# Kernel optimization log

Hardware: AMD Instinct MI355X
Metric: run time of the kernel (lower is better)

Reference implementation:

```python
import jax, jax.numpy as jnp
import numpy as np
from jax import lax

ALPHA = 50.0
BN_EPS = 1e-5
L2_EPS = 1e-12

N, C, H, W = 32, 128, 128, 128
K = 64  # num_clusters


def _l2norm(v, axis):
    n = jnp.sqrt(jnp.sum(v * v, axis=axis, keepdims=True))
    return v / jnp.maximum(n, L2_EPS)


def setup_inputs() -> dict:
    key = jax.random.key(0)
    ks = jax.random.split(key, 4)
    x = jax.random.normal(ks[0], (N, C, H, W), dtype=jnp.float32)
    conv_w = jax.random.normal(ks[1], (C, C, 3, 3), dtype=jnp.float32) * 0.05
    bn_gamma = jnp.ones((C,), jnp.float32)
    bn_beta = jnp.zeros((C,), jnp.float32)
    bn_mean = jnp.zeros((C,), jnp.float32)
    bn_var = jnp.ones((C,), jnp.float32)
    # conv.weight in NetVLAD is centroids.permute(1,0): shape (dim, num_clusters)
    vlad_w = jax.random.normal(ks[2], (C, K), dtype=jnp.float32)
    vlad_b = jnp.zeros((K,), jnp.float32)  # initialized to zeros in _init_params
    return {"input": x, "conv_w": conv_w, "bn_gamma": bn_gamma, "bn_beta": bn_beta,
            "bn_mean": bn_mean, "bn_var": bn_var, "vlad_w": vlad_w, "vlad_b": vlad_b,
            "norm_flag": 1}


def reference(input, conv_w, bn_gamma, bn_beta, bn_mean, bn_var, vlad_w, vlad_b, norm_flag):
    # bottleneck_layer_2: conv3x3 stride2 pad1 (no bias) -> BN (eval form) -> ReLU
    f = lax.conv_general_dilated(input, conv_w, window_strides=(2, 2),
                                 padding=[(1, 1), (1, 1)],
                                 dimension_numbers=("NCHW", "OIHW", "NCHW"))
    inv = bn_gamma / jnp.sqrt(bn_var + BN_EPS)
    f = f * inv[None, :, None, None] + (bn_beta - bn_mean * inv)[None, :, None, None]
    f = jax.nn.relu(f)

    n, c, h, w = f.shape
    hw = h * w
    # normalize_input: L2 over channel dim
    xn = _l2norm(f, axis=1)
    xf = xn.reshape(n, c, hw)  # (N,C,HW)

    # soft assignment: x^T @ normalize(W, dim=0), bias added, softmax over clusters
    wn = _l2norm(vlad_w, axis=0)                     # (C,K)
    sa_ = jnp.einsum("nci,ck->nik", xf, wn)          # (N,HW,K)
    logits = jnp.swapaxes(sa_, 1, 2) + vlad_b[None, :, None]  # (N,K,HW)
    a = jax.nn.softmax(ALPHA * logits, axis=1)       # softmax over K

    # vlad_k = sum_i a_ki * x_i - (sum_i a_ki) * c_k  (c_k = vlad_w[:,k], unnormalized)
    asum = jnp.sum(a, axis=-1)                       # (N,K)
    vlad = jnp.einsum("nki,nci->nkc", a, xf) - asum[:, :, None] * vlad_w.T[None]  # (N,K,C)

    vlad = _l2norm(vlad, axis=2)                     # intra-normalization
    vlad = vlad.reshape(n, -1)
    vlad = _l2norm(vlad, axis=1)

    feature = jnp.swapaxes(xf, 1, 2)                 # (N,HW,C)
    soft_assign_out = jnp.swapaxes(sa_, 1, 2)        # (N,K,HW)
    return (vlad, soft_assign_out, feature)
```

## Files before the change

kernel.cpp:

```cpp
#include <hip/hip_runtime.h>

typedef short short8 __attribute__((ext_vector_type(8)));
typedef float floatx4 __attribute__((ext_vector_type(4)));

#define ALPHA 50.0f
#define BN_EPS 1e-5f

#define SA_BASE   262144L
#define FEAT_BASE 8650752L

#define T_OFF    0L
#define AW_OFF   0L
#define PART_OFF 50331648L
#define XNT_OFF  138444800L
#define WB_OFF   171999232L
#define WNA_OFF  172294144L
#define ASUM_OFF 172310528L

__device__ __forceinline__ unsigned short f2bf(float f) {
    unsigned u = __builtin_bit_cast(unsigned, f);
    u = u + 0x7FFFu + ((u >> 16) & 1u);
    return (unsigned short)(u >> 16);
}

__device__ __forceinline__ void gl_lds16(const void* g, void* l) {
    __builtin_amdgcn_global_load_lds(
        (const __attribute__((address_space(1))) unsigned int*)g,
        (__attribute__((address_space(3))) unsigned int*)l, 16, 0, 0);
}

__global__ __launch_bounds__(256) void k_prep(const float* __restrict__ conv_w,
                                              const float* __restrict__ vlad_w,
                                              unsigned short* __restrict__ wB,
                                              unsigned short* __restrict__ wnA,
                                              float* __restrict__ asum) {
    int b = blockIdx.x, t = threadIdx.x;
    if (b < 576) {
        int idx = b * 256 + t;
        int ci = idx & 127, co = (idx >> 7) & 127, tap = idx >> 14;
        float w = conv_w[(co * 128 + ci) * 9 + tap];
        wB[(tap * 128 + co) * 128 + ci] = f2bf(w);
    } else {
        if (t < 64) {
            int k = t;
            float s = 0.0f;
            for (int c = 0; c < 128; c++) { float w = vlad_w[c * 64 + k]; s += w * w; }
            float rs = 1.0f / fmaxf(sqrtf(s), 1e-12f);
            for (int c = 0; c < 128; c++) wnA[k * 128 + c] = f2bf(vlad_w[c * 64 + k] * rs);
        } else {
            for (int i = t - 64; i < 2048; i += 192) asum[i] = 0.0f;
        }
    }
}

__global__ __launch_bounds__(256) void k_border(unsigned short* __restrict__ T) {
    int n = blockIdx.x, t = threadIdx.x;
    uint4 z = make_uint4(0, 0, 0, 0);
    for (int i = t; i < 4128; i += 256) {
        long e;
        if (i < 2080) {
            int ix = i >> 4, oct = i & 15;
            e = (((long)n * 130 + 0) * 130 + ix) * 128 + oct * 8;
        } else {
            int j = i - 2080;
            int row = (j >> 4) + 1, oct = j & 15;
            e = (((long)n * 130 + row) * 130 + 0) * 128 + oct * 8;
        }
        *(uint4*)(T + e) = z;
    }
}

__global__ __launch_bounds__(256) void k_xform(const float* __restrict__ in,
                                               unsigned short* __restrict__ T) {
    int y = blockIdx.x, n = blockIdx.y, t = threadIdx.x;
    __shared__ float ls[64 * 133];
    for (int cc = 0; cc < 2; cc++) {
        __syncthreads();
        int ci0 = cc * 64;
#pragma unroll
        for (int i = 0; i < 8; i++) {
            int idx = i * 256 + t;
            int ci = idx >> 5, xq = idx & 31;
            float4 v = *(const float4*)(in + ((((long)n * 128 + ci0 + ci) * 128 + y) * 128 + xq * 4));
            *(float4*)(&ls[ci * 133 + xq * 4]) = v;
        }
        __syncthreads();
#pragma unroll
        for (int i = 0; i < 4; i++) {
            int idx = i * 256 + t;
            int x = idx >> 3, oct = idx & 7;
            short8 pk;
#pragma unroll
            for (int j = 0; j < 8; j++)
                pk[j] = (short)f2bf(ls[(oct * 8 + j) * 133 + x]);
            long e = (((long)n * 130 + y + 1) * 130 + (x + 1)) * 128 + ci0 + oct * 8;
            *(short8*)(T + e) = pk;
        }
    }
}

__global__ __launch_bounds__(256) void k_conv(const unsigned short* __restrict__ T,
                                              const unsigned short* __restrict__ wB,
                                              const float* __restrict__ gamma,
                                              const float* __restrict__ beta,
                                              const float* __restrict__ mean,
                                              const float* __restrict__ var,
                                              float* __restrict__ out,
                                              unsigned short* __restrict__ xnT) {
    int ypair = blockIdx.x, n = blockIdx.y;
    int t = threadIdx.x, lane = t & 63, w = t >> 6;
    int wm = w >> 1, wn = w & 1;
    int s = lane & 15, q = lane >> 4;
    int y0 = ypair * 2;

    __shared__ __align__(16) short lsA[20800];
    __shared__ float lsq[256];

    floatx4 acc[4][4];
#pragma unroll
    for (int a = 0; a < 4; a++)
#pragma unroll
        for (int b = 0; b < 4; b++) acc[a][b] = (floatx4){0.f, 0.f, 0.f, 0.f};

    const unsigned short* Tbase = T + (((long)n * 130 + 2 * y0) * 130) * 128;
    int bbase0 = (wn * 64 + s) * 128 + q * 8;

    for (int cc = 0; cc < 4; cc++) {
        int ci0 = cc * 32;
        const unsigned short* Tc = Tbase + ci0;
#pragma unroll
        for (int i = 0; i < 11; i++) {
            int f = i * 256 + t;
            short* lbase = &lsA[2048 * i + 512 * w];
            if (f < 2600) {
                int r = f / 520;
                int rem = f - r * 520;
                int p = rem >> 3;
                int o8 = (rem & 7) ^ (p & 7);
                int ix = 2 * p + (o8 >> 2);
                int oct = o8 & 3;
                gl_lds16(Tc + (((long)(r * 130 + ix)) << 7) + (oct << 3), lbase);
            }
        }
        __syncthreads();
#pragma unroll
        for (int tap = 0; tap < 9; tap++) {
            const int dy = tap / 3, dx = tap % 3;
            short8 af[4], bf[4];
#pragma unroll
            for (int tm = 0; tm < 4; tm++) {
                int x = tm * 16 + s;
                int p = x + (dx >> 1);
                int o8p = (((dx & 1) << 2) | q) ^ (p & 7);
                int r = 2 * wm + dy;
                af[tm] = *(const short8*)(&lsA[(((r * 65 + p) << 3) + o8p) << 3]);
            }
#pragma unroll
            for (int tn = 0; tn < 4; tn++)
                bf[tn] = *(const short8*)(wB + bbase0 + tap * 16384 + tn * 2048 + ci0);
#pragma unroll
            for (int tm = 0; tm < 4; tm++)
#pragma unroll
                for (int tn = 0; tn < 4; tn++)
                    acc[tm][tn] = __builtin_amdgcn_mfma_f32_16x16x32_bf16(af[tm], bf[tn], acc[tm][tn], 0, 0, 0);
        }
        __syncthreads();
    }

    float inv[4], bt[4];
#pragma unroll
    for (int tn = 0; tn < 4; tn++) {
        int co = wn * 64 + tn * 16 + s;
        inv[tn] = gamma[co] / sqrtf(var[co] + BN_EPS);
        bt[tn] = beta[co] - mean[co] * inv[tn];
    }
#pragma unroll
    for (int tm = 0; tm < 4; tm++)
#pragma unroll
        for (int tn = 0; tn < 4; tn++)
#pragma unroll
            for (int r = 0; r < 4; r++) {
                float f = acc[tm][tn][r] * inv[tn] + bt[tn];
                acc[tm][tn][r] = fmaxf(f, 0.0f);
            }
#pragma unroll
    for (int tm = 0; tm < 4; tm++)
#pragma unroll
        for (int r = 0; r < 4; r++) {
            float p = 0.f;
#pragma unroll
            for (int tn = 0; tn < 4; tn++) { float f = acc[tm][tn][r]; p += f * f; }
            p += __shfl_xor(p, 1); p += __shfl_xor(p, 2);
            p += __shfl_xor(p, 4); p += __shfl_xor(p, 8);
            if (s == 0) lsq[wn * 128 + wm * 64 + tm * 16 + q * 4 + r] = p;
        }
    __syncthreads();
    float scl[4][4];
#pragma unroll
    for (int tm = 0; tm < 4; tm++)
#pragma unroll
        for (int r = 0; r < 4; r++) {
            int m = wm * 64 + tm * 16 + q * 4 + r;
            float tot = lsq[m] + lsq[128 + m];
            scl[tm][r] = 1.0f / fmaxf(sqrtf(tot), 1e-12f);
        }
    short* lsT = lsA;
    long pixbase = (long)n * 4096 + y0 * 64;
#pragma unroll
    for (int tm = 0; tm < 4; tm++)
#pragma unroll
        for (int r = 0; r < 4; r++) {
            int m = wm * 64 + tm * 16 + q * 4 + r;
#pragma unroll
            for (int tn = 0; tn < 4; tn++) {
                int co = wn * 64 + tn * 16 + s;
                float xv = acc[tm][tn][r] * scl[tm][r];
                out[FEAT_BASE + (pixbase + m) * 128 + co] = xv;
                lsT[co * 136 + m] = (short)f2bf(xv);
            }
        }
    __syncthreads();
    {
        int co = t >> 1, mh = t & 1;
        long base = ((long)n * 128 + co) * 4096 + y0 * 64 + mh * 64;
#pragma unroll
        for (int o = 0; o < 8; o++) {
            short8 v = *(short8*)(&lsT[co * 136 + mh * 64 + o * 8]);
            *(short8*)(xnT + base + o * 8) = v;
        }
    }
}

__global__ __launch_bounds__(256) void k_sa(const float* __restrict__ feat,
                                            const unsigned short* __restrict__ wnA,
                                            const float* __restrict__ vlad_b,
                                            float* __restrict__ out,
                                            unsigned short* __restrict__ aout,
                                            float* __restrict__ asum) {
    int pt = blockIdx.x, n = blockIdx.y;
    int t = threadIdx.x, lane = t & 63, w = t >> 6;
    int s = lane & 15, q = lane >> 4;
    int pb = pt * 256 + w * 64;

    floatx4 acc[4][4];
#pragma unroll
    for (int a = 0; a < 4; a++)
#pragma unroll
        for (int b = 0; b < 4; b++) acc[a][b] = (floatx4){0.f, 0.f, 0.f, 0.f};

    const float* fb = feat + FEAT_BASE + (long)n * 4096 * 128;
#pragma unroll
    for (int kk = 0; kk < 4; kk++) {
        int c0 = kk * 32 + q * 8;
        short8 af[4], bf[4];
#pragma unroll
        for (int tm = 0; tm < 4; tm++)
            af[tm] = *(const short8*)(wnA + (tm * 16 + s) * 128 + c0);
#pragma unroll
        for (int tn = 0; tn < 4; tn++) {
            const float* p = fb + (long)(pb + tn * 16 + s) * 128 + c0;
            float4 v0 = *(const float4*)p;
            float4 v1 = *(const float4*)(p + 4);
            short8 bv;
            bv[0] = (short)f2bf(v0.x); bv[1] = (short)f2bf(v0.y);
            bv[2] = (short)f2bf(v0.z); bv[3] = (short)f2bf(v0.w);
            bv[4] = (short)f2bf(v1.x); bv[5] = (short)f2bf(v1.y);
            bv[6] = (short)f2bf(v1.z); bv[7] = (short)f2bf(v1.w);
            bf[tn] = bv;
        }
#pragma unroll
        for (int tm = 0; tm < 4; tm++)
#pragma unroll
            for (int tn = 0; tn < 4; tn++)
                acc[tm][tn] = __builtin_amdgcn_mfma_f32_16x16x32_bf16(af[tm], bf[tn], acc[tm][tn], 0, 0, 0);
    }
    long sabase = SA_BASE + (long)n * 64 * 4096;
#pragma unroll
    for (int tm = 0; tm < 4; tm++)
#pragma unroll
        for (int r = 0; r < 4; r++) {
            int k = tm * 16 + q * 4 + r;
#pragma unroll
            for (int tn = 0; tn < 4; tn++)
                out[sabase + (long)k * 4096 + pb + tn * 16 + s] = acc[tm][tn][r];
        }
    float bv[4][4];
#pragma unroll
    for (int tm = 0; tm < 4; tm++)
#pragma unroll
        for (int r = 0; r < 4; r++) bv[tm][r] = vlad_b[tm * 16 + q * 4 + r];
#pragma unroll
    for (int tn = 0; tn < 4; tn++) {
        float M = -1e30f;
#pragma unroll
        for (int tm = 0; tm < 4; tm++)
#pragma unroll
            for (int r = 0; r < 4; r++)
                M = fmaxf(M, ALPHA * (acc[tm][tn][r] + bv[tm][r]));
        M = fmaxf(M, __shfl_xor(M, 16)); M = fmaxf(M, __shfl_xor(M, 32));
        float S = 0.f;
#pragma unroll
        for (int tm = 0; tm < 4; tm++)
#pragma unroll
            for (int r = 0; r < 4; r++) {
                float p = expf(ALPHA * (acc[tm][tn][r] + bv[tm][r]) - M);
                acc[tm][tn][r] = p; S += p;
            }
        S += __shfl_xor(S, 16); S += __shfl_xor(S, 32);
        float rS = 1.0f / S;
#pragma unroll
        for (int tm = 0; tm < 4; tm++)
#pragma unroll
            for (int r = 0; r < 4; r++) acc[tm][tn][r] *= rS;
    }
    long abase = (long)n * 64 * 4096;
#pragma unroll
    for (int tm = 0; tm < 4; tm++)
#pragma unroll
        for (int r = 0; r < 4; r++) {
            int k = tm * 16 + q * 4 + r;
#pragma unroll
            for (int tn = 0; tn < 4; tn++)
                aout[abase + (long)k * 4096 + pb + tn * 16 + s] = f2bf(acc[tm][tn][r]);
            float p = acc[tm][0][r] + acc[tm][1][r] + acc[tm][2][r] + acc[tm][3][r];
            p += __shfl_xor(p, 1); p += __shfl_xor(p, 2);
            p += __shfl_xor(p, 4); p += __shfl_xor(p, 8);
            if (s == 0) atomicAdd(asum + n * 64 + k, p);
        }
}

__global__ __launch_bounds__(256) void k_vlad1(const unsigned short* __restrict__ aw,
                                               const unsigned short* __restrict__ xnT,
                                               float* __restrict__ part) {
    int ch = blockIdx.x, n = blockIdx.y;
    int t = threadIdx.x, lane = t & 63, w = t >> 6;
    int wm = w >> 1, wn = w & 1;
    int s = lane & 15, q = lane >> 4;

    floatx4 acc[2][4];
#pragma unroll
    for (int a = 0; a < 2; a++)
#pragma unroll
        for (int b = 0; b < 4; b++) acc[a][b] = (floatx4){0.f, 0.f, 0.f, 0.f};

    const unsigned short* ab = aw + (long)n * 64 * 4096;
    const unsigned short* xb = xnT + (long)n * 128 * 4096;
    int ibeg = ch * 256, iend = ibeg + 256;
    for (int i0 = ibeg; i0 < iend; i0 += 32) {
        short8 af[2], bf[4];
#pragma unroll
        for (int tm = 0; tm < 2; tm++)
            af[tm] = *(const short8*)(ab + (long)(wm * 32 + tm * 16 + s) * 4096 + i0 + q * 8);
#pragma unroll
        for (int tn = 0; tn < 4; tn++)
            bf[tn] = *(const short8*)(xb + (long)(wn * 64 + tn * 16 + s) * 4096 + i0 + q * 8);
#pragma unroll
        for (int tm = 0; tm < 2; tm++)
#pragma unroll
            for (int tn = 0; tn < 4; tn++)
                acc[tm][tn] = __builtin_amdgcn_mfma_f32_16x16x32_bf16(af[tm], bf[tn], acc[tm][tn], 0, 0, 0);
    }
    float* pb = part + ((long)n * 16 + ch) * 8192;
#pragma unroll
    for (int tm = 0; tm < 2; tm++)
#pragma unroll
        for (int r = 0; r < 4; r++) {
            int k = wm * 32 + tm * 16 + q * 4 + r;
#pragma unroll
            for (int tn = 0; tn < 4; tn++) {
                int c = wn * 64 + tn * 16 + s;
                pb[k * 128 + c] = acc[tm][tn][r];
            }
        }
}

__global__ __launch_bounds__(256) void k_vlad2(const float* __restrict__ part,
                                               const float* __restrict__ vlad_w,
                                               const float* __restrict__ asum,
                                               float* __restrict__ out) {
    int n = blockIdx.x;
    int t = threadIdx.x, lane = t & 63, w = t >> 6;
    __shared__ float lsq[128];
    __shared__ float gsq[4];

    float v[32];
    const float* pb = part + (long)n * 16 * 8192;
#pragma unroll
    for (int j = 0; j < 32; j++) {
        int e = j * 256 + t;
        float sacc = 0.f;
#pragma unroll
        for (int c8 = 0; c8 < 16; c8++) sacc += pb[c8 * 8192 + e];
        int k = e >> 7, c = e & 127;
        sacc -= asum[n * 64 + k] * vlad_w[c * 64 + k];
        v[j] = sacc;
        float p = sacc * sacc;
        p += __shfl_xor(p, 1); p += __shfl_xor(p, 2); p += __shfl_xor(p, 4);
        p += __shfl_xor(p, 8); p += __shfl_xor(p, 16); p += __shfl_xor(p, 32);
        if (lane == 0) lsq[j * 4 + w] = p;
    }
    __syncthreads();
    float gp = 0.f;
#pragma unroll
    for (int j = 0; j < 32; j++) {
        float tot = lsq[j * 4 + (w & 2)] + lsq[j * 4 + (w & 2) + 1];
        float sc = 1.0f / fmaxf(sqrtf(tot), 1e-12f);
        v[j] *= sc;
        gp += v[j] * v[j];
    }
    gp += __shfl_xor(gp, 1); gp += __shfl_xor(gp, 2); gp += __shfl_xor(gp, 4);
    gp += __shfl_xor(gp, 8); gp += __shfl_xor(gp, 16); gp += __shfl_xor(gp, 32);
    if (lane == 0) gsq[w] = gp;
    __syncthreads();
    float sc2 = 1.0f / fmaxf(sqrtf(gsq[0] + gsq[1] + gsq[2] + gsq[3]), 1e-12f);
#pragma unroll
    for (int j = 0; j < 32; j++)
        out[(long)n * 8192 + j * 256 + t] = v[j] * sc2;
}

extern "C" void kernel_launch(void* const* d_in, const int* in_sizes, int n_in,
                              void* d_out, int out_size, void* d_ws, size_t ws_size,
                              hipStream_t stream) {
    const float* input  = (const float*)d_in[0];
    const float* conv_w = (const float*)d_in[1];
    const float* gamma  = (const float*)d_in[2];
    const float* beta   = (const float*)d_in[3];
    const float* mean   = (const float*)d_in[4];
    const float* var    = (const float*)d_in[5];
    const float* vlad_w = (const float*)d_in[6];
    const float* vlad_b = (const float*)d_in[7];
    float* out = (float*)d_out;
    char* ws = (char*)d_ws;

    unsigned short* T   = (unsigned short*)(ws + T_OFF);
    unsigned short* aw  = (unsigned short*)(ws + AW_OFF);
    float* part         = (float*)(ws + PART_OFF);
    unsigned short* xnT = (unsigned short*)(ws + XNT_OFF);
    unsigned short* wB  = (unsigned short*)(ws + WB_OFF);
    unsigned short* wnA = (unsigned short*)(ws + WNA_OFF);
    float* asum         = (float*)(ws + ASUM_OFF);

    k_prep<<<577, 256, 0, stream>>>(conv_w, vlad_w, wB, wnA, asum);
    k_border<<<32, 256, 0, stream>>>(T);
    k_xform<<<dim3(128, 32), 256, 0, stream>>>(input, T);
    k_conv<<<dim3(32, 32), 256, 0, stream>>>(T, wB, gamma, beta, mean, var, out, xnT);
    k_sa<<<dim3(16, 32), 256, 0, stream>>>(out, wnA, vlad_b, out, aw, asum);
    k_vlad1<<<dim3(16, 32), 256, 0, stream>>>(aw, xnT, part);
    k_vlad2<<<32, 256, 0, stream>>>(part, vlad_w, asum, out);
}
```

Baseline: 610.8 us.

## Fuse soft-assignment and VLAD aggregation into conv kernel epilogue

The soft-assignment GEMM, softmax, asum accumulation and per-tile VLAD partial GEMM now run inside the conv kernel on the normalized features already held in LDS, replacing the separate k_sa and k_vlad1 kernels. This removes the global round trips for the feature reread, the bf16 assignment matrix and the transposed feature copy, along with two launches. In exchange the conv kernel uses more LDS and registers, which may lower occupancy, and the partial buffer doubles to 32 slices per image, so k_vlad2 does a longer reduction.

```diff
diff --git a/kernel.cpp b/kernel.cpp
--- a/kernel.cpp
+++ b/kernel.cpp
@@ -10,9 +10,7 @@
 #define FEAT_BASE 8650752L
 
 #define T_OFF    0L
-#define AW_OFF   0L
-#define PART_OFF 50331648L
-#define XNT_OFF  138444800L
+#define PART_OFF 138444800L
 #define WB_OFF   171999232L
 #define WNA_OFF  172294144L
 #define ASUM_OFF 172310528L
@@ -105,15 +103,18 @@
                                               const float* __restrict__ beta,
                                               const float* __restrict__ mean,
                                               const float* __restrict__ var,
+                                              const unsigned short* __restrict__ wnA,
+                                              const float* __restrict__ vlad_b,
                                               float* __restrict__ out,
-                                              unsigned short* __restrict__ xnT) {
+                                              float* __restrict__ part,
+                                              float* __restrict__ asum) {
     int ypair = blockIdx.x, n = blockIdx.y;
     int t = threadIdx.x, lane = t & 63, w = t >> 6;
     int wm = w >> 1, wn = w & 1;
     int s = lane & 15, q = lane >> 4;
     int y0 = ypair * 2;
 
-    __shared__ __align__(16) short lsA[20800];
+    __shared__ __align__(16) short lsA[26112];
     __shared__ float lsq[256];
 
     floatx4 acc[4][4];
@@ -220,157 +221,120 @@
             }
         }
     __syncthreads();
-    {
-        int co = t >> 1, mh = t & 1;
-        long base = ((long)n * 128 + co) * 4096 + y0 * 64 + mh * 64;
-#pragma unroll
-        for (int o = 0; o < 8; o++) {
-            short8 v = *(short8*)(&lsT[co * 136 + mh * 64 + o * 8]);
-            *(short8*)(xnT + base + o * 8) = v;
-        }
-    }
-}
-
-__global__ __launch_bounds__(256) void k_sa(const float* __restrict__ feat,
-                                            const unsigned short* __restrict__ wnA,
-                                            const float* __restrict__ vlad_b,
-                                            float* __restrict__ out,
-                                            unsigned short* __restrict__ aout,
-                                            float* __restrict__ asum) {
-    int pt = blockIdx.x, n = blockIdx.y;
-    int t = threadIdx.x, lane = t & 63, w = t >> 6;
-    int s = lane & 15, q = lane >> 4;
-    int pb = pt * 256 + w * 64;
-
-    floatx4 acc[4][4];
+
+    floatx4 acc2[4][2];
 #pragma unroll
     for (int a = 0; a < 4; a++)
 #pragma unroll
-        for (int b = 0; b < 4; b++) acc[a][b] = (floatx4){0.f, 0.f, 0.f, 0.f};
-
-    const float* fb = feat + FEAT_BASE + (long)n * 4096 * 128;
+        for (int b = 0; b < 2; b++) acc2[a][b] = (floatx4){0.f, 0.f, 0.f, 0.f};
+    int pixw = w * 32;
 #pragma unroll
     for (int kk = 0; kk < 4; kk++) {
         int c0 = kk * 32 + q * 8;
-        short8 af[4], bf[4];
+        short8 af2[4], bf2[2];
 #pragma unroll
         for (int tm = 0; tm < 4; tm++)
-            af[tm] = *(const short8*)(wnA + (tm * 16 + s) * 128 + c0);
-#pragma unroll
-        for (int tn = 0; tn < 4; tn++) {
-            const float* p = fb + (long)(pb + tn * 16 + s) * 128 + c0;
-            float4 v0 = *(const float4*)p;
-            float4 v1 = *(const float4*)(p + 4);
+            af2[tm] = *(const short8*)(wnA + (tm * 16 + s) * 128 + c0);
+#pragma unroll
+        for (int tn = 0; tn < 2; tn++) {
+            int pix = pixw + tn * 16 + s;
             short8 bv;
-            bv[0] = (short)f2bf(v0.x); bv[1] = (short)f2bf(v0.y);
-            bv[2] = (short)f2bf(v0.z); bv[3] = (short)f2bf(v0.w);
-            bv[4] = (short)f2bf(v1.x); bv[5] = (short)f2bf(v1.y);
-            bv[6] = (short)f2bf(v1.z); bv[7] = (short)f2bf(v1.w);
-            bf[tn] = bv;
+#pragma unroll
+            for (int j = 0; j < 8; j++)
+                bv[j] = lsT[(c0 + j) * 136 + pix];
+            bf2[tn] = bv;
         }
 #pragma unroll
         for (int tm = 0; tm < 4; tm++)
 #pragma unroll
-            for (int tn = 0; tn < 4; tn++)
-                acc[tm][tn] = __builtin_amdgcn_mfma_f32_16x16x32_bf16(af[tm], bf[tn], acc[tm][tn], 0, 0, 0);
-    }
-    long sabase = SA_BASE + (long)n * 64 * 4096;
+            for (int tn = 0; tn < 2; tn++)
+                acc2[tm][tn] = __builtin_amdgcn_mfma_f32_16x16x32_bf16(af2[tm], bf2[tn], acc2[tm][tn], 0, 0, 0);
+    }
+    long sabase = SA_BASE + (long)n * 262144 + (long)(y0 * 64 + pixw);
 #pragma unroll
     for (int tm = 0; tm < 4; tm++)
 #pragma unroll
         for (int r = 0; r < 4; r++) {
             int k = tm * 16 + q * 4 + r;
 #pragma unroll
-            for (int tn = 0; tn < 4; tn++)
-                out[sabase + (long)k * 4096 + pb + tn * 16 + s] = acc[tm][tn][r];
-        }
-    float bv[4][4];
-#pragma unroll
-    for (int tm = 0; tm < 4; tm++)
-#pragma unroll
-        for (int r = 0; r < 4; r++) bv[tm][r] = vlad_b[tm * 16 + q * 4 + r];
-#pragma unroll
-    for (int tn = 0; tn < 4; tn++) {
+            for (int tn = 0; tn < 2; tn++)
+                out[sabase + (long)k * 4096 + tn * 16 + s] = acc2[tm][tn][r];
+        }
+    float bv2[4][4];
+#pragma unroll
+    for (int tm = 0; tm < 4; tm++)
+#pragma unroll
+        for (int r = 0; r < 4; r++) bv2[tm][r] = vlad_b[tm * 16 + q * 4 + r];
+#pragma unroll
+    for (int tn = 0; tn < 2; tn++) {
         float M = -1e30f;
 #pragma unroll
         for (int tm = 0; tm < 4; tm++)
 #pragma unroll
             for (int r = 0; r < 4; r++)
-                M = fmaxf(M, ALPHA * (acc[tm][tn][r] + bv[tm][r]));
+                M = fmaxf(M, ALPHA * (acc2[tm][tn][r] + bv2[tm][r]));
         M = fmaxf(M, __shfl_xor(M, 16)); M = fmaxf(M, __shfl_xor(M, 32));
         float S = 0.f;
 #pragma unroll
         for (int tm = 0; tm < 4; tm++)
 #pragma unroll
             for (int r = 0; r < 4; r++) {
-                float p = expf(ALPHA * (acc[tm][tn][r] + bv[tm][r]) - M);
-                acc[tm][tn][r] = p; S += p;
+                float p = expf(ALPHA * (acc2[tm][tn][r] + bv2[tm][r]) - M);
+                acc2[tm][tn][r] = p; S += p;
             }
         S += __shfl_xor(S, 16); S += __shfl_xor(S, 32);
         float rS = 1.0f / S;
 #pragma unroll
         for (int tm = 0; tm < 4; tm++)
 #pragma unroll
-            for (int r = 0; r < 4; r++) acc[tm][tn][r] *= rS;
-    }
-    long abase = (long)n * 64 * 4096;
+            for (int r = 0; r < 4; r++) acc2[tm][tn][r] *= rS;
+    }
+    short* lsAa = lsA + 17408;
 #pragma unroll
     for (int tm = 0; tm < 4; tm++)
 #pragma unroll
         for (int r = 0; r < 4; r++) {
             int k = tm * 16 + q * 4 + r;
 #pragma unroll
-            for (int tn = 0; tn < 4; tn++)
-                aout[abase + (long)k * 4096 + pb + tn * 16 + s] = f2bf(acc[tm][tn][r]);
-            float p = acc[tm][0][r] + acc[tm][1][r] + acc[tm][2][r] + acc[tm][3][r];
+            for (int tn = 0; tn < 2; tn++)
+                lsAa[k * 136 + pixw + tn * 16 + s] = (short)f2bf(acc2[tm][tn][r]);
+            float p = acc2[tm][0][r] + acc2[tm][1][r];
             p += __shfl_xor(p, 1); p += __shfl_xor(p, 2);
             p += __shfl_xor(p, 4); p += __shfl_xor(p, 8);
             if (s == 0) atomicAdd(asum + n * 64 + k, p);
         }
-}
-
-__global__ __launch_bounds__(256) void k_vlad1(const unsigned short* __restrict__ aw,
-                                               const unsigned short* __restrict__ xnT,
-                                               float* __restrict__ part) {
-    int ch = blockIdx.x, n = blockIdx.y;
-    int t = threadIdx.x, lane = t & 63, w = t >> 6;
-    int wm = w >> 1, wn = w & 1;
-    int s = lane & 15, q = lane >> 4;
-
-    floatx4 acc[2][4];
+    __syncthreads();
+    floatx4 acc3[2][4];
 #pragma unroll
     for (int a = 0; a < 2; a++)
 #pragma unroll
-        for (int b = 0; b < 4; b++) acc[a][b] = (floatx4){0.f, 0.f, 0.f, 0.f};
-
-    const unsigned short* ab = aw + (long)n * 64 * 4096;
-    const unsigned short* xb = xnT + (long)n * 128 * 4096;
-    int ibeg = ch * 256, iend = ibeg + 256;
-    for (int i0 = ibeg; i0 < iend; i0 += 32) {
-        short8 af[2], bf[4];
-#pragma unroll
-        for (int tm = 0; tm < 2; tm++)
-            af[tm] = *(const short8*)(ab + (long)(wm * 32 + tm * 16 + s) * 4096 + i0 + q * 8);
-#pragma unroll
-        for (int tn = 0; tn < 4; tn++)
-            bf[tn] = *(const short8*)(xb + (long)(wn * 64 + tn * 16 + s) * 4096 + i0 + q * 8);
-#pragma unroll
-        for (int tm = 0; tm < 2; tm++)
-#pragma unroll
-            for (int tn = 0; tn < 4; tn++)
-                acc[tm][tn] = __builtin_amdgcn_mfma_f32_16x16x32_bf16(af[tm], bf[tn], acc[tm][tn], 0, 0, 0);
-    }
-    float* pb = part + ((long)n * 16 + ch) * 8192;
-#pragma unroll
-    for (int tm = 0; tm < 2; tm++)
-#pragma unroll
-        for (int r = 0; r < 4; r++) {
-            int k = wm * 32 + tm * 16 + q * 4 + r;
-#pragma unroll
-            for (int tn = 0; tn < 4; tn++) {
-                int c = wn * 64 + tn * 16 + s;
-                pb[k * 128 + c] = acc[tm][tn][r];
-            }
+        for (int b = 0; b < 4; b++) acc3[a][b] = (floatx4){0.f, 0.f, 0.f, 0.f};
+    int kh = (w >> 1) * 32, ch0 = (w & 1) * 64;
+#pragma unroll
+    for (int pc = 0; pc < 4; pc++) {
+        int p0 = pc * 32 + q * 8;
+        short8 aA[2], bB[4];
+#pragma unroll
+        for (int tk = 0; tk < 2; tk++)
+            aA[tk] = *(const short8*)(lsAa + (kh + tk * 16 + s) * 136 + p0);
+#pragma unroll
+        for (int tc = 0; tc < 4; tc++)
+            bB[tc] = *(const short8*)(lsT + (ch0 + tc * 16 + s) * 136 + p0);
+#pragma unroll
+        for (int tk = 0; tk < 2; tk++)
+#pragma unroll
+            for (int tc = 0; tc < 4; tc++)
+                acc3[tk][tc] = __builtin_amdgcn_mfma_f32_16x16x32_bf16(aA[tk], bB[tc], acc3[tk][tc], 0, 0, 0);
+    }
+    float* pp = part + ((long)n * 32 + ypair) * 8192;
+#pragma unroll
+    for (int tk = 0; tk < 2; tk++)
+#pragma unroll
+        for (int r = 0; r < 4; r++) {
+            int k = kh + tk * 16 + q * 4 + r;
+#pragma unroll
+            for (int tc = 0; tc < 4; tc++)
+                pp[k * 128 + ch0 + tc * 16 + s] = acc3[tk][tc][r];
         }
 }
 
@@ -384,13 +348,13 @@
     __shared__ float gsq[4];
 
     float v[32];
-    const float* pb = part + (long)n * 16 * 8192;
+    const float* pb = part + (long)n * 32 * 8192;
 #pragma unroll
     for (int j = 0; j < 32; j++) {
         int e = j * 256 + t;
         float sacc = 0.f;
-#pragma unroll
-        for (int c8 = 0; c8 < 16; c8++) sacc += pb[c8 * 8192 + e];
+#pragma unroll 8
+        for (int c8 = 0; c8 < 32; c8++) sacc += pb[c8 * 8192 + e];
         int k = e >> 7, c = e & 127;
         sacc -= asum[n * 64 + k] * vlad_w[c * 64 + k];
         v[j] = sacc;
@@ -433,9 +397,7 @@
     char* ws = (char*)d_ws;
 
     unsigned short* T   = (unsigned short*)(ws + T_OFF);
-    unsigned short* aw  = (unsigned short*)(ws + AW_OFF);
     float* part         = (float*)(ws + PART_OFF);
-    unsigned short* xnT = (unsigned short*)(ws + XNT_OFF);
     unsigned short* wB  = (unsigned short*)(ws + WB_OFF);
     unsigned short* wnA = (unsigned short*)(ws + WNA_OFF);
     float* asum         = (float*)(ws + ASUM_OFF);
@@ -443,8 +405,6 @@
     k_prep<<<577, 256, 0, stream>>>(conv_w, vlad_w, wB, wnA, asum);
     k_border<<<32, 256, 0, stream>>>(T);
     k_xform<<<dim3(128, 32), 256, 0, stream>>>(input, T);
-    k_conv<<<dim3(32, 32), 256, 0, stream>>>(T, wB, gamma, beta, mean, var, out, xnT);
-    k_sa<<<dim3(16, 32), 256, 0, stream>>>(out, wnA, vlad_b, out, aw, asum);
-    k_vlad1<<<dim3(16, 32), 256, 0, stream>>>(aw, xnT, part);
+    k_conv<<<dim3(32, 32), 256, 0, stream>>>(T, wB, gamma, beta, mean, var, wnA, vlad_b, out, part, asum);
     k_vlad2<<<32, 256, 0, stream>>>(part, vlad_w, asum, out);
 }
```

Measured after the change: 640.2 us. 4.8% more time.
